# Kernel optimization log

Hardware: AMD Instinct MI355X
Metric: run time of the kernel (lower is better)

The kernel has to match this reference:

```python
import jax, jax.numpy as jnp
import numpy as np

ALPHA = 0.2  # LeakyReLU negative slope
NEG_INF = -9e15


def setup_inputs() -> dict:
    key = jax.random.key(0)
    k1, k2, k3, k4 = jax.random.split(key, 4)
    B, T, N, F_in, F_out = 8, 8, 1024, 64, 64
    h = jax.random.normal(k1, (B, T, N, F_in), dtype=jnp.float32)
    adj = jax.random.randint(k2, (B, T, N, N), 0, 2, dtype=jnp.int32)
    # xavier_uniform with gain=1.414
    def xavier(k, shape, gain=1.414):
        fan_in, fan_out = shape[0], shape[1]
        bound = gain * np.sqrt(6.0 / (fan_in + fan_out))
        return jax.random.uniform(k, shape, jnp.float32, -bound, bound)
    W = xavier(k3, (F_in, F_out))
    a = xavier(k4, (2 * F_out, 1))
    return {"h": h, "adj": adj, "W": W, "a": a}


def reference(h, adj, W, a):
    # h: [B,T,N,F_in], adj: [B,T,N,N], W: [F_in,F_out], a: [2*F_out,1]
    F_out = W.shape[1]
    Wh = h @ W  # [B,T,N,F_out]
    a1 = a[:F_out, 0]   # source half
    a2 = a[F_out:, 0]   # target half
    s1 = Wh @ a1        # [B,T,N]
    s2 = Wh @ a2        # [B,T,N]
    # e[...,i,j] = LeakyReLU(s1_i + s2_j)  == original concat-linear score
    e = jax.nn.leaky_relu(s1[..., :, None] + s2[..., None, :], negative_slope=ALPHA)
    att = jnp.where(adj > 0, e, NEG_INF)
    att = jax.nn.softmax(att, axis=-1)  # [B,T,N,N]
    # dropout omitted: reference runs in eval mode (p only active in training)
    h_prime = att @ Wh  # [B,T,N,F_out]
    return jax.nn.elu(h_prime)  # concat=True path
```

## Files before the change

### kernel.cpp

```cpp
#include <hip/hip_runtime.h>

#define NN 1024
#define FF 64
#define NBT 64

typedef float f32x4 __attribute__((ext_vector_type(4)));
typedef short s16x8 __attribute__((ext_vector_type(8)));

__device__ __forceinline__ short f2bf(float f) {
    unsigned u = __builtin_bit_cast(unsigned, f);
    u = (u + 0x7FFFu + ((u >> 16) & 1u)) >> 16;
    return (short)u;
}

__global__ __launch_bounds__(256) void k1(const float* __restrict__ h,
                                          const float* __restrict__ W,
                                          const float* __restrict__ a,
                                          short* __restrict__ WhT,
                                          float* __restrict__ s1g,
                                          float* __restrict__ s2g) {
    __shared__ float Wl[64 * 64];
    __shared__ float al[128];
    __shared__ float s1sh[128], s2sh[128];
    const int blk = blockIdx.x;
    const int bt = blk >> 3;
    const int rbase = (blk & 7) * 128;
    const int t = threadIdx.x;

    for (int i = t; i < 1024; i += 256)
        ((f32x4*)Wl)[i] = ((const f32x4*)W)[i];
    if (t < 32) ((f32x4*)al)[t] = ((const f32x4*)a)[t];
    __syncthreads();

    const int row = rbase + (t & 127);
    const int half = t >> 7;
    const float* hrow = h + ((size_t)bt * NN + row) * FF;
    float hv[64];
#pragma unroll
    for (int i = 0; i < 16; i++)
        ((f32x4*)hv)[i] = ((const f32x4*)hrow)[i];

    float s1 = 0.f, s2 = 0.f;
    short* wt = WhT + (size_t)bt * FF * NN + row;
#pragma unroll
    for (int cgi = 0; cgi < 8; cgi++) {
        const int cg = half * 8 + cgi;
        f32x4 acc = {0.f, 0.f, 0.f, 0.f};
#pragma unroll
        for (int k = 0; k < 64; k++) {
            f32x4 w4 = ((const f32x4*)Wl)[k * 16 + cg];
            acc += hv[k] * w4;
        }
        const int c0 = cg * 4;
        s1 += acc.x * al[c0] + acc.y * al[c0 + 1] + acc.z * al[c0 + 2] + acc.w * al[c0 + 3];
        s2 += acc.x * al[64 + c0] + acc.y * al[64 + c0 + 1] + acc.z * al[64 + c0 + 2] + acc.w * al[64 + c0 + 3];
        wt[(size_t)(c0 + 0) * NN] = f2bf(acc.x);
        wt[(size_t)(c0 + 1) * NN] = f2bf(acc.y);
        wt[(size_t)(c0 + 2) * NN] = f2bf(acc.z);
        wt[(size_t)(c0 + 3) * NN] = f2bf(acc.w);
    }
    if (half == 1) { s1sh[t & 127] = s1; s2sh[t & 127] = s2; }
    __syncthreads();
    if (half == 0) {
        s1g[bt * NN + row] = s1 + s1sh[t];
        s2g[bt * NN + row] = s2 + s2sh[t];
    }
}

__global__ __launch_bounds__(256) void k2(const int* __restrict__ adj,
                                          const short* __restrict__ WhT,
                                          const float* __restrict__ s1g,
                                          const float* __restrict__ s2g,
                                          float* __restrict__ out) {
    __shared__ __align__(16) short Pa[64 * 40];
    __shared__ __align__(16) short Pw[64 * 40];
    __shared__ float s2l[NN];
    __shared__ float rsum[64];

    const int bx = blockIdx.x;
    const int bt = bx >> 4;
    const int ibase = (bx & 15) * 64;
    const int t = threadIdx.x;

    ((f32x4*)s2l)[t] = ((const f32x4*)(s2g + bt * NN))[t];

    const int r = t >> 2;
    const int jc = (t & 3) * 8;
    const float s1v = s1g[bt * NN + ibase + r];
    float rs = 0.f;

    const int* adjp = adj + ((size_t)bt * NN + ibase + r) * NN + jc;
    const short* whp = WhT + (size_t)bt * FF * NN + (size_t)r * NN + jc;

    const int wv = t >> 6;
    const int l = t & 63;
    const int m = l & 15;
    const int q = l >> 4;
    const s16x8* aptr = (const s16x8*)&Pa[(wv * 16 + m) * 40 + q * 8];
    const s16x8* bp0 = (const s16x8*)&Pw[(0 * 16 + m) * 40 + q * 8];
    const s16x8* bp1 = (const s16x8*)&Pw[(1 * 16 + m) * 40 + q * 8];
    const s16x8* bp2 = (const s16x8*)&Pw[(2 * 16 + m) * 40 + q * 8];
    const s16x8* bp3 = (const s16x8*)&Pw[(3 * 16 + m) * 40 + q * 8];

    f32x4 acc0 = {0.f, 0.f, 0.f, 0.f};
    f32x4 acc1 = {0.f, 0.f, 0.f, 0.f};
    f32x4 acc2 = {0.f, 0.f, 0.f, 0.f};
    f32x4 acc3 = {0.f, 0.f, 0.f, 0.f};

    int4 ca0 = *(const int4*)(adjp);
    int4 ca1 = *(const int4*)(adjp + 4);
    int4 cw  = *(const int4*)(whp);

    __syncthreads();

    for (int jt = 0; jt < 32; jt++) {
        const int jn = (jt < 31) ? jt + 1 : 31;
        int4 na0 = *(const int4*)(adjp + jn * 32);
        int4 na1 = *(const int4*)(adjp + jn * 32 + 4);
        int4 nw  = *(const int4*)(whp + jn * 32);

        int aj[8] = {ca0.x, ca0.y, ca0.z, ca0.w, ca1.x, ca1.y, ca1.z, ca1.w};
        f32x4 s2a = *(const f32x4*)&s2l[jt * 32 + jc];
        f32x4 s2b = *(const f32x4*)&s2l[jt * 32 + jc + 4];
        float sv[8] = {s2a.x, s2a.y, s2a.z, s2a.w, s2b.x, s2b.y, s2b.z, s2b.w};
        s16x8 pbv;
#pragma unroll
        for (int u = 0; u < 8; u++) {
            float e = s1v + sv[u];
            e = e > 0.f ? e : 0.2f * e;
            e = fminf(e, 60.f);
            float p = (aj[u] > 0) ? __expf(e) : 0.f;
            rs += p;
            pbv[u] = f2bf(p);
        }
        *(s16x8*)&Pa[r * 40 + jc] = pbv;
        *(int4*)&Pw[r * 40 + jc] = cw;
        __syncthreads();

        s16x8 af = *aptr;
        acc0 = __builtin_amdgcn_mfma_f32_16x16x32_bf16(af, *bp0, acc0, 0, 0, 0);
        acc1 = __builtin_amdgcn_mfma_f32_16x16x32_bf16(af, *bp1, acc1, 0, 0, 0);
        acc2 = __builtin_amdgcn_mfma_f32_16x16x32_bf16(af, *bp2, acc2, 0, 0, 0);
        acc3 = __builtin_amdgcn_mfma_f32_16x16x32_bf16(af, *bp3, acc3, 0, 0, 0);
        __syncthreads();

        ca0 = na0; ca1 = na1; cw = nw;
    }

    rs += __shfl_xor(rs, 1);
    rs += __shfl_xor(rs, 2);
    if ((t & 3) == 0) rsum[r] = rs;
    __syncthreads();

    float rinv[4];
#pragma unroll
    for (int e = 0; e < 4; e++) {
        float rv = rsum[wv * 16 + q * 4 + e];
        rinv[e] = rv > 0.f ? 1.f / rv : 0.f;
    }
    float* outp = out + ((size_t)bt * NN + ibase + wv * 16 + q * 4) * FF + m;
#pragma unroll
    for (int e = 0; e < 4; e++) {
        float v0 = acc0[e] * rinv[e];
        float v1 = acc1[e] * rinv[e];
        float v2 = acc2[e] * rinv[e];
        float v3 = acc3[e] * rinv[e];
        v0 = v0 > 0.f ? v0 : expm1f(v0);
        v1 = v1 > 0.f ? v1 : expm1f(v1);
        v2 = v2 > 0.f ? v2 : expm1f(v2);
        v3 = v3 > 0.f ? v3 : expm1f(v3);
        float* o = outp + (size_t)e * FF;
        o[0]  = v0;
        o[16] = v1;
        o[32] = v2;
        o[48] = v3;
    }
}

extern "C" void kernel_launch(void* const* d_in, const int* in_sizes, int n_in,
                              void* d_out, int out_size, void* d_ws, size_t ws_size,
                              hipStream_t stream) {
    const float* h  = (const float*)d_in[0];
    const int*  adj = (const int*)d_in[1];
    const float* W  = (const float*)d_in[2];
    const float* a  = (const float*)d_in[3];
    float* out = (float*)d_out;

    short* WhT = (short*)d_ws;
    float* s1  = (float*)((char*)d_ws + (size_t)NBT * FF * NN * 2);
    float* s2  = s1 + NBT * NN;

    k1<<<512, 256, 0, stream>>>(h, W, a, WhT, s1, s2);
    k2<<<1024, 256, 0, stream>>>(adj, WhT, s1, s2, out);
}
```

Measured before the change: 415.4 us.

## Compute attention probabilities directly in MFMA register layout, drop LDS staging

Each lane now computes the exp-scores for the A-fragment positions it feeds to MFMA and loads WhT B-fragments straight from global memory. This removes the per-tile LDS writes and both __syncthreads barriers. Each wave now handles 32 rows (two A fragments) with 8 accumulators, halving the grid to 512 blocks. Row sums are reduced with lane shuffles instead of shared memory, and ELU uses __expf-1 instead of expm1f. The cost is more registers, lower occupancy, and redundant global reads of WhT across waves, which were previously shared through LDS.

```diff
diff --git a/kernel.cpp b/kernel.cpp
--- a/kernel.cpp
+++ b/kernel.cpp
@@ -72,108 +72,118 @@
                                           const float* __restrict__ s1g,
                                           const float* __restrict__ s2g,
                                           float* __restrict__ out) {
-    __shared__ __align__(16) short Pa[64 * 40];
-    __shared__ __align__(16) short Pw[64 * 40];
     __shared__ float s2l[NN];
-    __shared__ float rsum[64];
 
     const int bx = blockIdx.x;
-    const int bt = bx >> 4;
-    const int ibase = (bx & 15) * 64;
+    const int bt = bx >> 3;
+    const int ib = (bx & 7) * 128;
     const int t = threadIdx.x;
-
-    ((f32x4*)s2l)[t] = ((const f32x4*)(s2g + bt * NN))[t];
-
-    const int r = t >> 2;
-    const int jc = (t & 3) * 8;
-    const float s1v = s1g[bt * NN + ibase + r];
-    float rs = 0.f;
-
-    const int* adjp = adj + ((size_t)bt * NN + ibase + r) * NN + jc;
-    const short* whp = WhT + (size_t)bt * FF * NN + (size_t)r * NN + jc;
-
     const int wv = t >> 6;
     const int l = t & 63;
     const int m = l & 15;
     const int q = l >> 4;
-    const s16x8* aptr = (const s16x8*)&Pa[(wv * 16 + m) * 40 + q * 8];
-    const s16x8* bp0 = (const s16x8*)&Pw[(0 * 16 + m) * 40 + q * 8];
-    const s16x8* bp1 = (const s16x8*)&Pw[(1 * 16 + m) * 40 + q * 8];
-    const s16x8* bp2 = (const s16x8*)&Pw[(2 * 16 + m) * 40 + q * 8];
-    const s16x8* bp3 = (const s16x8*)&Pw[(3 * 16 + m) * 40 + q * 8];
-
-    f32x4 acc0 = {0.f, 0.f, 0.f, 0.f};
-    f32x4 acc1 = {0.f, 0.f, 0.f, 0.f};
-    f32x4 acc2 = {0.f, 0.f, 0.f, 0.f};
-    f32x4 acc3 = {0.f, 0.f, 0.f, 0.f};
-
-    int4 ca0 = *(const int4*)(adjp);
-    int4 ca1 = *(const int4*)(adjp + 4);
-    int4 cw  = *(const int4*)(whp);
+
+    ((f32x4*)s2l)[t] = ((const f32x4*)(s2g + bt * NN))[t];
+
+    const int r0 = ib + wv * 32 + m;
+    const int r1 = r0 + 16;
+    const float s1a = s1g[bt * NN + r0];
+    const float s1b = s1g[bt * NN + r1];
+
+    const int* ap0 = adj + ((size_t)bt * NN + r0) * NN + q * 8;
+    const int* ap1 = adj + ((size_t)bt * NN + r1) * NN + q * 8;
+    const short* wb = WhT + (size_t)bt * FF * NN + q * 8;
+    const short* bq0 = wb + (size_t)(0 * 16 + m) * NN;
+    const short* bq1 = wb + (size_t)(1 * 16 + m) * NN;
+    const short* bq2 = wb + (size_t)(2 * 16 + m) * NN;
+    const short* bq3 = wb + (size_t)(3 * 16 + m) * NN;
+
+    f32x4 acc[8];
+#pragma unroll
+    for (int i = 0; i < 8; i++) acc[i] = (f32x4){0.f, 0.f, 0.f, 0.f};
+    float rs0 = 0.f, rs1 = 0.f;
+
+    int4 ca00 = *(const int4*)(ap0);
+    int4 ca01 = *(const int4*)(ap0 + 4);
+    int4 ca10 = *(const int4*)(ap1);
+    int4 ca11 = *(const int4*)(ap1 + 4);
+    s16x8 cb0 = *(const s16x8*)(bq0);
+    s16x8 cb1 = *(const s16x8*)(bq1);
+    s16x8 cb2 = *(const s16x8*)(bq2);
+    s16x8 cb3 = *(const s16x8*)(bq3);
 
     __syncthreads();
 
     for (int jt = 0; jt < 32; jt++) {
-        const int jn = (jt < 31) ? jt + 1 : 31;
-        int4 na0 = *(const int4*)(adjp + jn * 32);
-        int4 na1 = *(const int4*)(adjp + jn * 32 + 4);
-        int4 nw  = *(const int4*)(whp + jn * 32);
-
-        int aj[8] = {ca0.x, ca0.y, ca0.z, ca0.w, ca1.x, ca1.y, ca1.z, ca1.w};
-        f32x4 s2a = *(const f32x4*)&s2l[jt * 32 + jc];
-        f32x4 s2b = *(const f32x4*)&s2l[jt * 32 + jc + 4];
-        float sv[8] = {s2a.x, s2a.y, s2a.z, s2a.w, s2b.x, s2b.y, s2b.z, s2b.w};
-        s16x8 pbv;
+        const int off = (jt < 31 ? jt + 1 : 31) * 32;
+        int4 na00 = *(const int4*)(ap0 + off);
+        int4 na01 = *(const int4*)(ap0 + off + 4);
+        int4 na10 = *(const int4*)(ap1 + off);
+        int4 na11 = *(const int4*)(ap1 + off + 4);
+        s16x8 nb0 = *(const s16x8*)(bq0 + off);
+        s16x8 nb1 = *(const s16x8*)(bq1 + off);
+        s16x8 nb2 = *(const s16x8*)(bq2 + off);
+        s16x8 nb3 = *(const s16x8*)(bq3 + off);
+
+        f32x4 s2a = *(const f32x4*)&s2l[jt * 32 + q * 8];
+        f32x4 s2b = *(const f32x4*)&s2l[jt * 32 + q * 8 + 4];
+        const float sv[8] = {s2a.x, s2a.y, s2a.z, s2a.w, s2b.x, s2b.y, s2b.z, s2b.w};
+
+        const int aj0[8] = {ca00.x, ca00.y, ca00.z, ca00.w, ca01.x, ca01.y, ca01.z, ca01.w};
+        const int aj1[8] = {ca10.x, ca10.y, ca10.z, ca10.w, ca11.x, ca11.y, ca11.z, ca11.w};
+        s16x8 pa0, pa1;
 #pragma unroll
         for (int u = 0; u < 8; u++) {
-            float e = s1v + sv[u];
-            e = e > 0.f ? e : 0.2f * e;
-            e = fminf(e, 60.f);
-            float p = (aj[u] > 0) ? __expf(e) : 0.f;
-            rs += p;
-            pbv[u] = f2bf(p);
+            float e0 = s1a + sv[u];
+            e0 = fmaxf(e0, 0.2f * e0);
+            e0 = fminf(e0, 60.f);
+            float p0 = (aj0[u] > 0) ? __expf(e0) : 0.f;
+            rs0 += p0;
+            pa0[u] = f2bf(p0);
+
+            float e1 = s1b + sv[u];
+            e1 = fmaxf(e1, 0.2f * e1);
+            e1 = fminf(e1, 60.f);
+            float p1 = (aj1[u] > 0) ? __expf(e1) : 0.f;
+            rs1 += p1;
+            pa1[u] = f2bf(p1);
         }
-        *(s16x8*)&Pa[r * 40 + jc] = pbv;
-        *(int4*)&Pw[r * 40 + jc] = cw;
-        __syncthreads();
-
-        s16x8 af = *aptr;
-        acc0 = __builtin_amdgcn_mfma_f32_16x16x32_bf16(af, *bp0, acc0, 0, 0, 0);
-        acc1 = __builtin_amdgcn_mfma_f32_16x16x32_bf16(af, *bp1, acc1, 0, 0, 0);
-        acc2 = __builtin_amdgcn_mfma_f32_16x16x32_bf16(af, *bp2, acc2, 0, 0, 0);
-        acc3 = __builtin_amdgcn_mfma_f32_16x16x32_bf16(af, *bp3, acc3, 0, 0, 0);
-        __syncthreads();
-
-        ca0 = na0; ca1 = na1; cw = nw;
-    }
-
-    rs += __shfl_xor(rs, 1);
-    rs += __shfl_xor(rs, 2);
-    if ((t & 3) == 0) rsum[r] = rs;
-    __syncthreads();
-
-    float rinv[4];
+
+        acc[0] = __builtin_amdgcn_mfma_f32_16x16x32_bf16(pa0, cb0, acc[0], 0, 0, 0);
+        acc[1] = __builtin_amdgcn_mfma_f32_16x16x32_bf16(pa0, cb1, acc[1], 0, 0, 0);
+        acc[2] = __builtin_amdgcn_mfma_f32_16x16x32_bf16(pa0, cb2, acc[2], 0, 0, 0);
+        acc[3] = __builtin_amdgcn_mfma_f32_16x16x32_bf16(pa0, cb3, acc[3], 0, 0, 0);
+        acc[4] = __builtin_amdgcn_mfma_f32_16x16x32_bf16(pa1, cb0, acc[4], 0, 0, 0);
+        acc[5] = __builtin_amdgcn_mfma_f32_16x16x32_bf16(pa1, cb1, acc[5], 0, 0, 0);
+        acc[6] = __builtin_amdgcn_mfma_f32_16x16x32_bf16(pa1, cb2, acc[6], 0, 0, 0);
+        acc[7] = __builtin_amdgcn_mfma_f32_16x16x32_bf16(pa1, cb3, acc[7], 0, 0, 0);
+
+        ca00 = na00; ca01 = na01; ca10 = na10; ca11 = na11;
+        cb0 = nb0; cb1 = nb1; cb2 = nb2; cb3 = nb3;
+    }
+
+    rs0 += __shfl_xor(rs0, 16);
+    rs0 += __shfl_xor(rs0, 32);
+    rs1 += __shfl_xor(rs1, 16);
+    rs1 += __shfl_xor(rs1, 32);
+
+    float* ob = out + ((size_t)bt * NN + ib + wv * 32) * FF + m;
 #pragma unroll
     for (int e = 0; e < 4; e++) {
-        float rv = rsum[wv * 16 + q * 4 + e];
-        rinv[e] = rv > 0.f ? 1.f / rv : 0.f;
-    }
-    float* outp = out + ((size_t)bt * NN + ibase + wv * 16 + q * 4) * FF + m;
-#pragma unroll
-    for (int e = 0; e < 4; e++) {
-        float v0 = acc0[e] * rinv[e];
-        float v1 = acc1[e] * rinv[e];
-        float v2 = acc2[e] * rinv[e];
-        float v3 = acc3[e] * rinv[e];
-        v0 = v0 > 0.f ? v0 : expm1f(v0);
-        v1 = v1 > 0.f ? v1 : expm1f(v1);
-        v2 = v2 > 0.f ? v2 : expm1f(v2);
-        v3 = v3 > 0.f ? v3 : expm1f(v3);
-        float* o = outp + (size_t)e * FF;
-        o[0]  = v0;
-        o[16] = v1;
-        o[32] = v2;
-        o[48] = v3;
+        const int ro = q * 4 + e;
+        float rA = __shfl(rs0, ro);
+        float rB = __shfl(rs1, ro);
+        float iA = rA > 0.f ? 1.f / rA : 0.f;
+        float iB = rB > 0.f ? 1.f / rB : 0.f;
+#pragma unroll
+        for (int cg = 0; cg < 4; cg++) {
+            float v = acc[cg][e] * iA;
+            v = v > 0.f ? v : (__expf(v) - 1.f);
+            ob[(size_t)ro * FF + cg * 16] = v;
+            float w = acc[4 + cg][e] * iB;
+            w = w > 0.f ? w : (__expf(w) - 1.f);
+            ob[(size_t)(16 + ro) * FF + cg * 16] = w;
+        }
     }
 }
 
@@ -191,5 +201,5 @@
     float* s2  = s1 + NBT * NN;
 
     k1<<<512, 256, 0, stream>>>(h, W, a, WhT, s1, s2);
-    k2<<<1024, 256, 0, stream>>>(adj, WhT, s1, s2, out);
-}
+    k2<<<512, 256, 0, stream>>>(adj, WhT, s1, s2, out);
+}
```

New measurement: 418.9 us. No clear change (+0.8%).
